# Kernel tuning notes

Measured on AMD Instinct MI355X. Metric: run time of the kernel, lower is better.

## Reference

```python
import jax, jax.numpy as jnp
import numpy as np
from jax import lax

B, W, K = 64, 128, 64      # batch, window_size, n_features
KS = 7                      # conv kernel size
EF = W                      # feature-attn embed dim (defaults to window_size, GATv1)
ET = 2 * K                  # temporal-attn embed dim (n_features doubled by GATv2)
H = 256                     # GRU hidden
FH = 256                    # forecast MLP hidden
ALPHA = 0.2                 # leaky relu slope


def _leaky(v):
    return jnp.where(v >= 0, v, ALPHA * v)


def setup_inputs() -> dict:
    key = jax.random.key(0)
    ks = jax.random.split(key, 20)
    s = 0.05
    inp = {
        "x": jax.random.normal(ks[0], (B, W, K), jnp.float32),
        # ConvLayer
        "conv_w": jax.random.normal(ks[1], (K, K, KS), jnp.float32) * s,
        "conv_b": jnp.zeros((K,), jnp.float32),
        # FeatureAttentionLayer (GATv1): lin W->EF, a:[2EF,1], bias [K,K]
        "feat_lin_w": jax.random.normal(ks[2], (EF, W), jnp.float32) * s,
        "feat_lin_b": jnp.zeros((EF,), jnp.float32),
        "feat_a": jax.random.normal(ks[3], (2 * EF, 1), jnp.float32) * s,
        "feat_bias": jnp.zeros((K, K), jnp.float32),
        # TemporalAttentionLayer (GATv2): lin 2K->ET, a:[ET,1], bias [W,W]
        "temp_lin_w": jax.random.normal(ks[4], (ET, 2 * K), jnp.float32) * s,
        "temp_lin_b": jnp.zeros((ET,), jnp.float32),
        "temp_a": jax.random.normal(ks[5], (ET, 1), jnp.float32) * s,
        "temp_bias": jnp.zeros((W, W), jnp.float32),
        # GRU (1 layer), input dim 3K
        "gru_wih": jax.random.normal(ks[6], (3 * H, 3 * K), jnp.float32) * s,
        "gru_whh": jax.random.normal(ks[7], (3 * H, H), jnp.float32) * s,
        "gru_bih": jnp.zeros((3 * H,), jnp.float32),
        "gru_bhh": jnp.zeros((3 * H,), jnp.float32),
        "fc0_w": jax.random.normal(ks[8], (FH, H), jnp.float32) * s,
        "fc0_b": jnp.zeros((FH,), jnp.float32),
        "fc1_w": jax.random.normal(ks[9], (FH, FH), jnp.float32) * s,
        "fc1_b": jnp.zeros((FH,), jnp.float32),
        "fc2_w": jax.random.normal(ks[10], (FH, FH), jnp.float32) * s,
        "fc2_b": jnp.zeros((FH,), jnp.float32),
        "fc3_w": jax.random.normal(ks[11], (K, FH), jnp.float32) * s,
        "fc3_b": jnp.zeros((K,), jnp.float32),
    }
    return inp


def _forward(x, conv_w, conv_b, feat_lin_w, feat_lin_b, feat_a, feat_bias,
             temp_lin_w, temp_lin_b, temp_a, temp_bias,
             gru_wih, gru_whh, gru_bih, gru_bhh,
             fc0_w, fc0_b, fc1_w, fc1_b, fc2_w, fc2_b, fc3_w, fc3_b):
    # --- ConvLayer: pad (k-1)//2 both sides, Conv1d K->K, ReLU ---
    pad = (KS - 1) // 2
    xc = x.transpose(0, 2, 1)                                   # [B,K,W]
    xc = jnp.pad(xc, ((0, 0), (0, 0), (pad, pad)))
    y = lax.conv_general_dilated(xc, conv_w, (1,), 'VALID',
                                 dimension_numbers=('NCH', 'OIH', 'NCH'))
    y = jax.nn.relu(y + conv_b[None, :, None]).transpose(0, 2, 1)  # [B,W,K]

    # --- FeatureAttentionLayer (GATv1): e_ij = leaky((Wx_i||Wx_j)·a) ---
    xf = y.transpose(0, 2, 1)                                   # [B,K,W]
    Wx = xf @ feat_lin_w.T + feat_lin_b                         # [B,K,EF]
    s1 = Wx @ feat_a[:EF, 0]                                    # [B,K]
    s2 = Wx @ feat_a[EF:, 0]                                    # [B,K]
    e_f = _leaky(s1[:, :, None] + s2[:, None, :]) + feat_bias   # [B,K,K]
    att_f = jax.nn.softmax(e_f, axis=2)
    h_feat = jax.nn.sigmoid(att_f @ xf).transpose(0, 2, 1)      # [B,W,K]

    # --- TemporalAttentionLayer (GATv2): g = leaky(lin(x_i||x_j)); e = g·a ---
    W1, W2 = temp_lin_w[:, :K], temp_lin_w[:, K:]               # split lin over concat halves
    p = y @ W1.T                                                # [B,W,ET]
    q = y @ W2.T                                                # [B,W,ET]
    g = _leaky(p[:, :, None, :] + q[:, None, :, :] + temp_lin_b)  # [B,W,W,ET]
    e_t = (g @ temp_a)[..., 0] + temp_bias                      # [B,W,W]
    att_t = jax.nn.softmax(e_t, axis=2)
    h_temp = jax.nn.sigmoid(att_t @ y)                          # [B,W,K]

    # --- concat + GRU over time ---
    z = jnp.concatenate([y, h_feat, h_temp], axis=2)            # [B,W,3K]

    def gru_step(h, xt):
        gi = xt @ gru_wih.T + gru_bih                           # [B,3H]
        gh = h @ gru_whh.T + gru_bhh
        ir, iz, inn = jnp.split(gi, 3, axis=1)
        hr, hz, hn = jnp.split(gh, 3, axis=1)
        r = jax.nn.sigmoid(ir + hr)
        zg = jax.nn.sigmoid(iz + hz)
        n = jnp.tanh(inn + r * hn)
        return (1.0 - zg) * n + zg * h, None

    h0 = jnp.zeros((z.shape[0], H), z.dtype)
    h_end, _ = lax.scan(gru_step, h0, z.transpose(1, 0, 2))     # [B,H]

    # --- Forecasting MLP (eval mode: dropout is identity) ---
    v = jax.nn.relu(h_end @ fc0_w.T + fc0_b)
    v = jax.nn.relu(v @ fc1_w.T + fc1_b)
    v = jax.nn.relu(v @ fc2_w.T + fc2_b)
    return v @ fc3_w.T + fc3_b                                  # [B,K]


def reference(x, conv_w, conv_b, feat_lin_w, feat_lin_b, feat_a, feat_bias,
              temp_lin_w, temp_lin_b, temp_a, temp_bias,
              gru_wih, gru_whh, gru_bih, gru_bhh,
              fc0_w, fc0_b, fc1_w, fc1_b, fc2_w, fc2_b, fc3_w, fc3_b):
    return _forward(x, conv_w, conv_b, feat_lin_w, feat_lin_b, feat_a, feat_bias,
                    temp_lin_w, temp_lin_b, temp_a, temp_bias,
                    gru_wih, gru_whh, gru_bih, gru_bhh,
                    fc0_w, fc0_b, fc1_w, fc1_b, fc2_w, fc2_b, fc3_w, fc3_b)
```

## Files before the change

### kernel.cpp

```cpp
#include <hip/hip_runtime.h>
#include <hip/hip_bf16.h>

typedef unsigned int uint;
typedef _Float16 half2_t __attribute__((ext_vector_type(2)));
typedef float f32x4 __attribute__((ext_vector_type(4)));
typedef uint u32x4 __attribute__((ext_vector_type(4)));

union H2U { uint u; half2_t h; };

#define OFF_Y    0u
#define OFF_Z    524288u
#define OFF_GI   2097152u
#define OFF_WHH  8388608u
#define OFF_C12  8486912u
#define OFF_DD   8487168u
#define OFF_HEND 8487424u

__global__ __launch_bounds__(256) void k_pack_prep(const float* __restrict__ whh, uint* __restrict__ w16,
                                                   const float* __restrict__ flw, const float* __restrict__ flb,
                                                   const float* __restrict__ fa, float* __restrict__ c12,
                                                   float* __restrict__ dd) {
    __shared__ float red[256];
    int bx = blockIdx.x, tid = threadIdx.x;
    if (bx < 384) {
        int idx = bx * 256 + tid;
        int tidq = idx / 192;
        int r = idx - tidq * 192;
        int u = r >> 5;
        int q = (r >> 2) & 7;
        int p = r & 3;
        int w = tidq >> 6;
        int l = tidq & 63;
        int row = w * 96 + u * 16 + (l & 15);
        int colb = q * 32 + (l >> 4) * 8 + 2 * p;
        float a = whh[(size_t)row * 256 + colb];
        float b = whh[(size_t)row * 256 + colb + 1];
        H2U uu; uu.h.x = (_Float16)a; uu.h.y = (_Float16)b;
        w16[idx] = uu.u;
    } else {
        if (tid < 128) {
            float a = 0.f, b = 0.f;
            for (int e = 0; e < 128; ++e) {
                float w = flw[e * 128 + tid];
                a = fmaf(w, fa[e], a);
                b = fmaf(w, fa[128 + e], b);
            }
            c12[tid] = a;
            c12[128 + tid] = b;
        }
        int e = tid & 127;
        red[tid] = (tid < 128) ? flb[e] * fa[e] : flb[e] * fa[128 + e];
        __syncthreads();
        if (tid < 2) {
            float s = 0.f;
            for (int q = 0; q < 128; ++q) s += red[tid * 128 + q];
            dd[tid] = s;
        }
    }
}

__global__ __launch_bounds__(256) void k_conv(const float* __restrict__ x, const float* __restrict__ cw,
                                              const float* __restrict__ cb, float* __restrict__ y,
                                              float* __restrict__ z) {
    __shared__ float xT[64][41];
    __shared__ float cwL[64 * 64 * 7];
    int b = blockIdx.y, w0 = blockIdx.x * 32, tid = threadIdx.x;
    for (int idx = tid; idx < 38 * 64; idx += 256) {
        int wl = idx / 64, k = idx % 64;
        int wg = w0 - 3 + wl;
        xT[k][wl] = (wg >= 0 && wg < 128) ? x[((size_t)b * 128 + wg) * 64 + k] : 0.f;
    }
    for (int idx = tid; idx < 64 * 64 * 7; idx += 256) cwL[idx] = cw[idx];
    __syncthreads();
    int w_l = tid % 32, kog = tid / 32;
    float acc[8];
#pragma unroll
    for (int i = 0; i < 8; ++i) acc[i] = 0.f;
    for (int ki = 0; ki < 64; ++ki) {
        float x7[7];
#pragma unroll
        for (int u = 0; u < 7; ++u) x7[u] = xT[ki][w_l + u];
#pragma unroll
        for (int koi = 0; koi < 8; ++koi) {
            const float* wp = &cwL[((kog * 8 + koi) * 64 + ki) * 7];
#pragma unroll
            for (int u = 0; u < 7; ++u) acc[koi] = fmaf(x7[u], wp[u], acc[koi]);
        }
    }
    int w = w0 + w_l;
#pragma unroll
    for (int koi = 0; koi < 8; ++koi) {
        int ko = kog * 8 + koi;
        float v = acc[koi] + cb[ko];
        v = v > 0.f ? v : 0.f;
        y[((size_t)b * 128 + w) * 64 + ko] = v;
        z[((size_t)b * 128 + w) * 192 + ko] = v;
    }
}

__global__ __launch_bounds__(256) void k_feat(const float* __restrict__ y, const float* __restrict__ c12,
                                              const float* __restrict__ dd, const float* __restrict__ fb,
                                              float* __restrict__ z) {
    int b = blockIdx.y, w0 = blockIdx.x * 32, tid = threadIdx.x;
    __shared__ float s1L[64], s2L[64];
    __shared__ float attL[64][65];
    __shared__ float yL[32][64];
    __shared__ float cL[256];
    cL[tid] = c12[tid];
    for (int idx = tid; idx < 32 * 64; idx += 256) {
        int wl = idx / 64, j = idx % 64;
        yL[wl][j] = y[((size_t)b * 128 + w0 + wl) * 64 + j];
    }
    __syncthreads();
    if (tid < 128) {
        int k = tid % 64;
        const float* c = (tid < 64) ? cL : cL + 128;
        float acc = 0.f;
        for (int w = 0; w < 128; ++w) acc = fmaf(y[((size_t)b * 128 + w) * 64 + k], c[w], acc);
        if (tid < 64) s1L[k] = acc + dd[0]; else s2L[k] = acc + dd[1];
    }
    __syncthreads();
    if (tid < 64) {
        int k = tid;
        float s1 = s1L[k];
        float m = -1e30f;
        for (int j = 0; j < 64; ++j) {
            float v = s1 + s2L[j];
            float l = fmaxf(v, 0.2f * v);
            float e = l + fb[k * 64 + j];
            attL[k][j] = e;
            m = fmaxf(m, e);
        }
        float s = 0.f;
        for (int j = 0; j < 64; ++j) { float e = __expf(attL[k][j] - m); attL[k][j] = e; s += e; }
        float inv = 1.f / s;
        for (int j = 0; j < 64; ++j) attL[k][j] *= inv;
    }
    __syncthreads();
    int k_l = tid % 64, wg = tid / 64;
    for (int wi = 0; wi < 8; ++wi) {
        int wl = wg * 8 + wi;
        float acc = 0.f;
#pragma unroll 16
        for (int j = 0; j < 64; ++j) acc = fmaf(attL[k_l][j], yL[wl][j], acc);
        float hv = 1.f / (1.f + __expf(-acc));
        z[((size_t)b * 128 + w0 + wl) * 192 + 64 + k_l] = hv;
    }
}

__global__ __launch_bounds__(512) void k_temp(const float* __restrict__ y, const float* __restrict__ tlw,
                                              const float* __restrict__ tlb, const float* __restrict__ ta,
                                              const float* __restrict__ tbias, float* __restrict__ z) {
    int b = blockIdx.y, i0 = blockIdx.x * 32, tid = threadIdx.x;
    __shared__ __align__(16) float yT[64][132];
    __shared__ __align__(16) float qL[128][132];
    __shared__ __align__(16) float pL[32][128];
    __shared__ __align__(16) float etL[32][128];
    __shared__ __align__(16) float taL[128];
    __shared__ float mred[32][8], sred[32][8];
    __shared__ float mrow[32], invL[32];
    if (tid < 128) taL[tid] = ta[tid];
    for (int idx = tid; idx < 8192; idx += 512) {
        int j = idx >> 6, k = idx & 63;
        yT[k][j] = y[((size_t)b * 128 + j) * 64 + k];
    }
    __syncthreads();
    {
        int c = tid & 127, ih = tid >> 7;
        float w1r[64];
        const float4* w1p = (const float4*)(tlw + c * 128);
#pragma unroll
        for (int q4 = 0; q4 < 16; ++q4) {
            float4 v = w1p[q4];
            w1r[4 * q4] = v.x; w1r[4 * q4 + 1] = v.y; w1r[4 * q4 + 2] = v.z; w1r[4 * q4 + 3] = v.w;
        }
        float base = tlb[c];
#pragma unroll
        for (int ilb = 0; ilb < 2; ++ilb) {
            int j0 = i0 + ih * 8 + ilb * 4;
            float4 acc = {base, base, base, base};
            for (int k = 0; k < 64; ++k) {
                float4 yv = *((const float4*)&yT[k][j0]);
                float w = w1r[k];
                acc.x = fmaf(yv.x, w, acc.x); acc.y = fmaf(yv.y, w, acc.y);
                acc.z = fmaf(yv.z, w, acc.z); acc.w = fmaf(yv.w, w, acc.w);
            }
            int il = ih * 8 + ilb * 4;
            pL[il][c] = acc.x; pL[il + 1][c] = acc.y; pL[il + 2][c] = acc.z; pL[il + 3][c] = acc.w;
        }
    }
    {
        int c = tid & 127, ih = tid >> 7;
        float w2r[64];
        const float4* w2p = (const float4*)(tlw + c * 128 + 64);
#pragma unroll
        for (int q4 = 0; q4 < 16; ++q4) {
            float4 v = w2p[q4];
            w2r[4 * q4] = v.x; w2r[4 * q4 + 1] = v.y; w2r[4 * q4 + 2] = v.z; w2r[4 * q4 + 3] = v.w;
        }
#pragma unroll
        for (int jq = 0; jq < 8; ++jq) {
            int j0 = ih * 32 + jq * 4;
            float4 acc = {0.f, 0.f, 0.f, 0.f};
            for (int k = 0; k < 64; ++k) {
                float4 yv = *((const float4*)&yT[k][j0]);
                float w = w2r[k];
                acc.x = fmaf(yv.x, w, acc.x); acc.y = fmaf(yv.y, w, acc.y);
                acc.z = fmaf(yv.z, w, acc.z); acc.w = fmaf(yv.w, w, acc.w);
            }
            *((float4*)&qL[c][j0]) = acc;
        }
    }
    __syncthreads();
    {
        int jg = tid & 31, ih = tid >> 5;
        int j0 = jg * 4;
        int il0 = ih * 2;
        float4 acc0 = *((const float4*)(tbias + (size_t)(i0 + il0) * 128 + j0));
        float4 acc1 = *((const float4*)(tbias + (size_t)(i0 + il0 + 1) * 128 + j0));
        for (int c0 = 0; c0 < 128; c0 += 4) {
            float4 ta4 = *((const float4*)&taL[c0]);
            float4 p0 = *((const float4*)&pL[il0][c0]);
            float4 p1 = *((const float4*)&pL[il0 + 1][c0]);
            float4 q0 = *((const float4*)&qL[c0 + 0][j0]);
            float4 q1 = *((const float4*)&qL[c0 + 1][j0]);
            float4 q2 = *((const float4*)&qL[c0 + 2][j0]);
            float4 q3 = *((const float4*)&qL[c0 + 3][j0]);
#define ETSTEP(qv, tac, pa, pb) { \
            float u; \
            u = (pa) + qv.x; acc0.x = fmaf(fmaxf(u, 0.2f * u), (tac), acc0.x); \
            u = (pa) + qv.y; acc0.y = fmaf(fmaxf(u, 0.2f * u), (tac), acc0.y); \
            u = (pa) + qv.z; acc0.z = fmaf(fmaxf(u, 0.2f * u), (tac), acc0.z); \
            u = (pa) + qv.w; acc0.w = fmaf(fmaxf(u, 0.2f * u), (tac), acc0.w); \
            u = (pb) + qv.x; acc1.x = fmaf(fmaxf(u, 0.2f * u), (tac), acc1.x); \
            u = (pb) + qv.y; acc1.y = fmaf(fmaxf(u, 0.2f * u), (tac), acc1.y); \
            u = (pb) + qv.z; acc1.z = fmaf(fmaxf(u, 0.2f * u), (tac), acc1.z); \
            u = (pb) + qv.w; acc1.w = fmaf(fmaxf(u, 0.2f * u), (tac), acc1.w); }
            ETSTEP(q0, ta4.x, p0.x, p1.x)
            ETSTEP(q1, ta4.y, p0.y, p1.y)
            ETSTEP(q2, ta4.z, p0.z, p1.z)
            ETSTEP(q3, ta4.w, p0.w, p1.w)
#undef ETSTEP
        }
        *((float4*)&etL[il0][j0]) = acc0;
        *((float4*)&etL[il0 + 1][j0]) = acc1;
    }
    __syncthreads();
    if (tid < 256) {
        int il = tid >> 3, seg = tid & 7;
        const float4* ep = (const float4*)&etL[il][seg * 16];
        float m = -1e30f;
#pragma unroll
        for (int q = 0; q < 4; ++q) {
            float4 e = ep[q];
            m = fmaxf(m, fmaxf(fmaxf(e.x, e.y), fmaxf(e.z, e.w)));
        }
        mred[il][seg] = m;
    }
    __syncthreads();
    if (tid < 32) {
        float m = mred[tid][0];
#pragma unroll
        for (int s = 1; s < 8; ++s) m = fmaxf(m, mred[tid][s]);
        mrow[tid] = m;
    }
    __syncthreads();
    if (tid < 256) {
        int il = tid >> 3, seg = tid & 7;
        float m = mrow[il];
        float4* ep = (float4*)&etL[il][seg * 16];
        float s = 0.f;
#pragma unroll
        for (int q = 0; q < 4; ++q) {
            float4 e = ep[q];
            e.x = __expf(e.x - m); e.y = __expf(e.y - m);
            e.z = __expf(e.z - m); e.w = __expf(e.w - m);
            s += (e.x + e.y) + (e.z + e.w);
            ep[q] = e;
        }
        sred[il][seg] = s;
    }
    __syncthreads();
    if (tid < 32) {
        float s = 0.f;
#pragma unroll
        for (int q = 0; q < 8; ++q) s += sred[tid][q];
        invL[tid] = 1.f / s;
    }
    __syncthreads();
    {
        int k = tid & 63, ig = tid >> 6;
        float acc[4] = {0.f, 0.f, 0.f, 0.f};
        const float* yb = y + (size_t)b * 128 * 64 + k;
        for (int j0 = 0; j0 < 128; j0 += 4) {
            float yv[4];
#pragma unroll
            for (int jj = 0; jj < 4; ++jj) yv[jj] = yb[(size_t)(j0 + jj) * 64];
#pragma unroll
            for (int ii = 0; ii < 4; ++ii) {
                int il = ig * 4 + ii;
                float4 ev = *((const float4*)&etL[il][j0]);
                acc[ii] = fmaf(ev.x, yv[0], acc[ii]);
                acc[ii] = fmaf(ev.y, yv[1], acc[ii]);
                acc[ii] = fmaf(ev.z, yv[2], acc[ii]);
                acc[ii] = fmaf(ev.w, yv[3], acc[ii]);
            }
        }
#pragma unroll
        for (int ii = 0; ii < 4; ++ii) {
            int il = ig * 4 + ii;
            float hv = 1.f / (1.f + __expf(-acc[ii] * invL[il]));
            z[((size_t)b * 128 + i0 + il) * 192 + 128 + k] = hv;
        }
    }
}

__global__ __launch_bounds__(256) void k_gi(const float* __restrict__ z, const float* __restrict__ wih,
                                            const float* __restrict__ bih, float* __restrict__ gi) {
    int o0 = blockIdx.x * 128;
    int bt0 = blockIdx.y * 64;
    int tid = threadIdx.x;
    __shared__ __align__(16) float zL[64][68];
    __shared__ float wL[128][65];
    int ol = tid & 31;
    int r8 = (tid >> 5) * 8;
    float acc[8][4];
#pragma unroll
    for (int rr = 0; rr < 8; ++rr)
#pragma unroll
        for (int oo = 0; oo < 4; ++oo) acc[rr][oo] = 0.f;
    for (int mc = 0; mc < 3; ++mc) {
        int m0 = mc * 64;
        __syncthreads();
        {
            int mq = (tid & 15) * 4;
            int r = tid >> 4;
#pragma unroll
            for (int it = 0; it < 4; ++it, r += 16) {
                float4 v = *((const float4*)&z[(size_t)(bt0 + r) * 192 + m0 + mq]);
                *((float4*)&zL[r][mq]) = v;
            }
            int o = tid >> 4;
#pragma unroll
            for (int it = 0; it < 8; ++it, o += 16) {
                float4 v = *((const float4*)&wih[(size_t)(o0 + o) * 192 + m0 + mq]);
                wL[o][mq] = v.x; wL[o][mq + 1] = v.y; wL[o][mq + 2] = v.z; wL[o][mq + 3] = v.w;
            }
        }
        __syncthreads();
        for (int mb = 0; mb < 64; mb += 4) {
            float4 zv[8];
#pragma unroll
            for (int rr = 0; rr < 8; ++rr) zv[rr] = *((const float4*)&zL[r8 + rr][mb]);
#pragma unroll
            for (int mi = 0; mi < 4; ++mi) {
                float wv[4];
#pragma unroll
                for (int oo = 0; oo < 4; ++oo) wv[oo] = wL[ol + 32 * oo][mb + mi];
#pragma unroll
                for (int rr = 0; rr < 8; ++rr) {
                    float zc = (mi == 0) ? zv[rr].x : (mi == 1) ? zv[rr].y : (mi == 2) ? zv[rr].z : zv[rr].w;
#pragma unroll
                    for (int oo = 0; oo < 4; ++oo) acc[rr][oo] = fmaf(zc, wv[oo], acc[rr][oo]);
                }
            }
        }
    }
    float bo[4];
#pragma unroll
    for (int oo = 0; oo < 4; ++oo) bo[oo] = bih[o0 + ol + 32 * oo];
#pragma unroll
    for (int rr = 0; rr < 8; ++rr)
#pragma unroll
        for (int oo = 0; oo < 4; ++oo)
            gi[(size_t)(bt0 + r8 + rr) * 768 + o0 + ol + 32 * oo] = acc[rr][oo] + bo[oo];
}

__global__ __launch_bounds__(512)
__attribute__((amdgpu_waves_per_eu(2, 2)))
void k_gru(const float* __restrict__ gi,
           const uint* __restrict__ w16,
           const float* __restrict__ bhh,
           float* __restrict__ hend) {
    int b = blockIdx.x, tid = threadIdx.x;
    int w = tid >> 6, l = tid & 63;
    int t = tid & 255;
    int quad = l >> 4;
    __shared__ __align__(16) _Float16 hp16[256];
    __shared__ float sH[768];
    u32x4 wq[48];
    {
        const u32x4* wp4 = (const u32x4*)(w16 + (size_t)tid * 192);
#pragma unroll
        for (int i = 0; i < 48; ++i) wq[i] = wp4[i];
    }
    float br = 0.f, bz = 0.f, bn = 0.f;
    if (tid < 256) { br = bhh[t]; bz = bhh[256 + t]; bn = bhh[512 + t]; }
    float h = 0.f;
    if (tid < 128) ((uint*)hp16)[tid] = 0u;
    __syncthreads();
    const float* gib = gi + (size_t)b * 128 * 768;
    const u32x4* hp4 = (const u32x4*)hp16;
    int sbase = w * 96 + l;
    for (int s = 0; s < 128; ++s) {
        float gr = 0.f, gz = 0.f, gn = 0.f;
        if (tid < 256) {
            gr = gib[s * 768 + t];
            gz = gib[s * 768 + 256 + t];
            gn = gib[s * 768 + 512 + t];
        }
        f32x4 acc[6];
#pragma unroll
        for (int u = 0; u < 6; ++u) acc[u] = (f32x4){0.f, 0.f, 0.f, 0.f};
#pragma unroll
        for (int q = 0; q < 8; ++q) {
            u32x4 avu = hp4[q * 4 + quad];
            asm volatile(
                "v_mfma_f32_16x16x32_f16 %0, %6, %7, %0\n\t"
                "v_mfma_f32_16x16x32_f16 %1, %6, %8, %1\n\t"
                "v_mfma_f32_16x16x32_f16 %2, %6, %9, %2\n\t"
                "v_mfma_f32_16x16x32_f16 %3, %6, %10, %3\n\t"
                "v_mfma_f32_16x16x32_f16 %4, %6, %11, %4\n\t"
                "v_mfma_f32_16x16x32_f16 %5, %6, %12, %5\n\t"
                "s_nop 7\n\t"
                "s_nop 7\n\t"
                : "+v"(acc[0]), "+v"(acc[1]), "+v"(acc[2]),
                  "+v"(acc[3]), "+v"(acc[4]), "+v"(acc[5])
                : "v"(avu),
                  "a"(wq[0 * 8 + q]), "a"(wq[1 * 8 + q]), "a"(wq[2 * 8 + q]),
                  "a"(wq[3 * 8 + q]), "a"(wq[4 * 8 + q]), "a"(wq[5 * 8 + q]));
        }
        if (l < 16) {
            sH[sbase +  0] = acc[0][0];
            sH[sbase + 16] = acc[1][0];
            sH[sbase + 32] = acc[2][0];
            sH[sbase + 48] = acc[3][0];
            sH[sbase + 64] = acc[4][0];
            sH[sbase + 80] = acc[5][0];
        }
        __syncthreads();
        if (tid < 256) {
            float hr = sH[t] + br;
            float hz = sH[256 + t] + bz;
            float hn = sH[512 + t] + bn;
            float r  = 1.f / (1.f + __expf(-(gr + hr)));
            float zg = 1.f / (1.f + __expf(-(gz + hz)));
            float nx = gn + r * hn;
            float n  = 1.f - 2.f / (1.f + __expf(2.f * nx));
            h = (1.f - zg) * n + zg * h;
            hp16[t] = (_Float16)h;
        }
        __syncthreads();
    }
    if (tid < 256) hend[b * 256 + t] = h;
}

__global__ __launch_bounds__(256) void k_fc(const float* __restrict__ hend,
                                            const float* __restrict__ w0, const float* __restrict__ b0,
                                            const float* __restrict__ w1, const float* __restrict__ b1,
                                            const float* __restrict__ w2, const float* __restrict__ b2,
                                            const float* __restrict__ w3, const float* __restrict__ b3,
                                            float* __restrict__ out) {
    int b = blockIdx.x, tid = threadIdx.x;
    __shared__ float bufA[256], bufB[256];
    bufA[tid] = hend[b * 256 + tid];
    __syncthreads();
    {
        float acc = b0[tid];
        const float* wrow = &w0[tid * 256];
#pragma unroll 8
        for (int m = 0; m < 256; ++m) acc = fmaf(wrow[m], bufA[m], acc);
        bufB[tid] = fmaxf(acc, 0.f);
    }
    __syncthreads();
    {
        float acc = b1[tid];
        const float* wrow = &w1[tid * 256];
#pragma unroll 8
        for (int m = 0; m < 256; ++m) acc = fmaf(wrow[m], bufB[m], acc);
        bufA[tid] = fmaxf(acc, 0.f);
    }
    __syncthreads();
    {
        float acc = b2[tid];
        const float* wrow = &w2[tid * 256];
#pragma unroll 8
        for (int m = 0; m < 256; ++m) acc = fmaf(wrow[m], bufA[m], acc);
        bufB[tid] = fmaxf(acc, 0.f);
    }
    __syncthreads();
    if (tid < 64) {
        float acc = b3[tid];
        const float* wrow = &w3[tid * 256];
#pragma unroll 8
        for (int m = 0; m < 256; ++m) acc = fmaf(wrow[m], bufB[m], acc);
        out[b * 64 + tid] = acc;
    }
}

extern "C" void kernel_launch(void* const* d_in, const int* in_sizes, int n_in,
                              void* d_out, int out_size, void* d_ws, size_t ws_size,
                              hipStream_t stream) {
    const float* x    = (const float*)d_in[0];
    const float* cw   = (const float*)d_in[1];
    const float* cb   = (const float*)d_in[2];
    const float* flw  = (const float*)d_in[3];
    const float* flb  = (const float*)d_in[4];
    const float* fa   = (const float*)d_in[5];
    const float* fb   = (const float*)d_in[6];
    const float* tlw  = (const float*)d_in[7];
    const float* tlb  = (const float*)d_in[8];
    const float* ta   = (const float*)d_in[9];
    const float* tb   = (const float*)d_in[10];
    const float* wih  = (const float*)d_in[11];
    const float* whh  = (const float*)d_in[12];
    const float* bih  = (const float*)d_in[13];
    const float* bhh  = (const float*)d_in[14];
    const float* fc0w = (const float*)d_in[15];
    const float* fc0b = (const float*)d_in[16];
    const float* fc1w = (const float*)d_in[17];
    const float* fc1b = (const float*)d_in[18];
    const float* fc2w = (const float*)d_in[19];
    const float* fc2b = (const float*)d_in[20];
    const float* fc3w = (const float*)d_in[21];
    const float* fc3b = (const float*)d_in[22];

    float* wsf  = (float*)d_ws;
    float* y    = wsf + OFF_Y;
    float* z    = wsf + OFF_Z;
    float* gi   = wsf + OFF_GI;
    uint*  w16  = (uint*)(wsf + OFF_WHH);
    float* c12  = wsf + OFF_C12;
    float* dd   = wsf + OFF_DD;
    float* hend = wsf + OFF_HEND;
    float* out  = (float*)d_out;

    k_pack_prep<<<385, 256, 0, stream>>>(whh, w16, flw, flb, fa, c12, dd);
    k_conv<<<dim3(4, 64), 256, 0, stream>>>(x, cw, cb, y, z);
    k_feat<<<dim3(4, 64), 256, 0, stream>>>(y, c12, dd, fb, z);
    k_temp<<<dim3(4, 64), 512, 0, stream>>>(y, tlw, tlb, ta, tb, z);
    k_gi<<<dim3(6, 128), 256, 0, stream>>>(z, wih, bih, gi);
    k_gru<<<64, 512, 0, stream>>>(gi, w16, bhh, hend);
    k_fc<<<64, 256, 0, stream>>>(hend, fc0w, fc0b, fc1w, fc1b, fc2w, fc2b, fc3w, fc3b, out);
}
```

Before: 434.8 us.

## Stream part of GRU recurrent weights from global memory instead of registers

Only four of the six per-wave MFMA weight tiles stay resident in AGPRs. The remaining two are repacked into a separate global region and reloaded each timestep with a one-step software prefetch. This lowers register pressure in the GRU recurrence, but adds global or L2 loads on the serial critical path of every step.

```diff
diff --git a/kernel.cpp b/kernel.cpp
--- a/kernel.cpp
+++ b/kernel.cpp
@@ -24,15 +24,26 @@
     int bx = blockIdx.x, tid = threadIdx.x;
     if (bx < 384) {
         int idx = bx * 256 + tid;
-        int tidq = idx / 192;
-        int r = idx - tidq * 192;
-        int u = r >> 5;
-        int q = (r >> 2) & 7;
-        int p = r & 3;
-        int w = tidq >> 6;
-        int l = tidq & 63;
-        int row = w * 96 + u * 16 + (l & 15);
-        int colb = q * 32 + (l >> 4) * 8 + 2 * p;
+        int row, colb, p;
+        if (idx < 65536) {
+            int tidq = idx >> 7;
+            int r = idx & 127;
+            int u = r >> 5;
+            int q = (r >> 2) & 7;
+            p = r & 3;
+            int w = tidq >> 6, l = tidq & 63;
+            row = w * 96 + u * 16 + (l & 15);
+            colb = q * 32 + (l >> 4) * 8 + 2 * p;
+        } else {
+            int idx2 = idx - 65536;
+            p = idx2 & 3;
+            int l = (idx2 >> 2) & 63;
+            int q = (idx2 >> 8) & 7;
+            int ut = (idx2 >> 11) & 1;
+            int w = idx2 >> 12;
+            row = w * 96 + (4 + ut) * 16 + (l & 15);
+            colb = q * 32 + (l >> 4) * 8 + 2 * p;
+        }
         float a = whh[(size_t)row * 256 + colb];
         float b = whh[(size_t)row * 256 + colb + 1];
         H2U uu; uu.h.x = (_Float16)a; uu.h.y = (_Float16)b;
@@ -388,12 +399,15 @@
     int quad = l >> 4;
     __shared__ __align__(16) _Float16 hp16[256];
     __shared__ float sH[768];
-    u32x4 wq[48];
-    {
-        const u32x4* wp4 = (const u32x4*)(w16 + (size_t)tid * 192);
-#pragma unroll
-        for (int i = 0; i < 48; ++i) wq[i] = wp4[i];
-    }
+    u32x4 wq[32];
+    {
+        const u32x4* wp4 = (const u32x4*)(w16 + (size_t)tid * 128);
+#pragma unroll
+        for (int i = 0; i < 32; ++i) wq[i] = wp4[i];
+    }
+    const u32x4* wg4 = (const u32x4*)(w16 + 65536);
+    const u32x4* st4 = wg4 + ((w * 2 + 0) * 8) * 64 + l;
+    const u32x4* st5 = wg4 + ((w * 2 + 1) * 8) * 64 + l;
     float br = 0.f, bz = 0.f, bn = 0.f;
     if (tid < 256) { br = bhh[t]; bz = bhh[256 + t]; bn = bhh[512 + t]; }
     float h = 0.f;
@@ -412,8 +426,11 @@
         f32x4 acc[6];
 #pragma unroll
         for (int u = 0; u < 6; ++u) acc[u] = (f32x4){0.f, 0.f, 0.f, 0.f};
+        u32x4 c4 = st4[0], c5 = st5[0];
 #pragma unroll
         for (int q = 0; q < 8; ++q) {
+            u32x4 n4, n5;
+            if (q < 7) { n4 = st4[(q + 1) * 64]; n5 = st5[(q + 1) * 64]; }
             u32x4 avu = hp4[q * 4 + quad];
             asm volatile(
                 "v_mfma_f32_16x16x32_f16 %0, %6, %7, %0\n\t"
@@ -427,8 +444,10 @@
                 : "+v"(acc[0]), "+v"(acc[1]), "+v"(acc[2]),
                   "+v"(acc[3]), "+v"(acc[4]), "+v"(acc[5])
                 : "v"(avu),
-                  "a"(wq[0 * 8 + q]), "a"(wq[1 * 8 + q]), "a"(wq[2 * 8 + q]),
-                  "a"(wq[3 * 8 + q]), "a"(wq[4 * 8 + q]), "a"(wq[5 * 8 + q]));
+                  "a"(wq[0 * 8 + q]), "a"(wq[1 * 8 + q]),
+                  "a"(wq[2 * 8 + q]), "a"(wq[3 * 8 + q]),
+                  "v"(c4), "v"(c5));
+            if (q < 7) { c4 = n4; c5 = n5; }
         }
         if (l < 16) {
             sH[sbase +  0] = acc[0][0];
```

Result: no change. 430.8 us (-0.9%).
